# Performance work log

Hardware: AMD Instinct MI355X
Metric: run time of the kernel (lower is better)

Reference implementation:

```python
import jax, jax.numpy as jnp
import numpy as np
import math

B, S, D, H, L, FF = 16, 512, 1024, 16, 4, 4096
DK = D // H
EPS = 1e-5
NEG = -1e32


def make_pe(max_len, d_model):
    pos = np.arange(max_len, dtype=np.float32)[:, None]
    div = np.exp(np.arange(0, d_model, 2, dtype=np.float32) * (-math.log(10000.0) / d_model))
    pe = np.zeros((max_len, d_model), dtype=np.float32)
    pe[:, 0::2] = np.sin(pos * div)
    pe[:, 1::2] = np.cos(pos * div)
    return jnp.asarray(pe[None])  # [1, max_len, d_model]


def setup_inputs() -> dict:
    key = jax.random.key(0)
    ks = jax.random.split(key, 32)
    sd = 0.02
    inp = {
        'q_embed_data': jax.random.normal(ks[0], (B, S, D), jnp.float32),
        'qa_embed_data': jax.random.normal(ks[1], (B, S, D), jnp.float32),
        'forget_rate': jax.random.uniform(ks[2], (B, 1, S, 1), jnp.float32),
        'pe': make_pe(S, D),
        'Wk': jax.random.normal(ks[3], (L, D, D), jnp.float32) * sd,
        'bk': jnp.zeros((L, D), jnp.float32),
        'Wv': jax.random.normal(ks[4], (L, D, D), jnp.float32) * sd,
        'bv': jnp.zeros((L, D), jnp.float32),
        'Wo': jax.random.normal(ks[5], (L, D, D), jnp.float32) * sd,
        'bo': jnp.zeros((L, D), jnp.float32),
        'W1': jax.random.normal(ks[6], (L, D, FF), jnp.float32) * sd,
        'b1': jnp.zeros((L, FF), jnp.float32),
        'W2': jax.random.normal(ks[7], (L, FF, D), jnp.float32) * sd,
        'b2': jnp.zeros((L, D), jnp.float32),
        'ln1_g': jnp.ones((L, D), jnp.float32),
        'ln1_b': jnp.zeros((L, D), jnp.float32),
        'ln2_g': jnp.ones((L, D), jnp.float32),
        'ln2_b': jnp.zeros((L, D), jnp.float32),
    }
    return inp


def layernorm(x, g, b):
    m = jnp.mean(x, -1, keepdims=True)
    v = jnp.mean((x - m) ** 2, -1, keepdims=True)
    return (x - m) * jax.lax.rsqrt(v + EPS) * g + b


def forward(q_embed_data, qa_embed_data, forget_rate, pe,
            Wk, bk, Wv, bv, Wo, bo, W1, b1, W2, b2,
            ln1_g, ln1_b, ln2_g, ln2_b):
    x = q_embed_data + pe[:, :S]
    y = qa_embed_data + pe[:, :S]
    # mask==0 path: allowed positions are strictly below diagonal (j < i)
    allowed = jnp.tril(jnp.ones((S, S), bool), k=-1)
    scale = 1.0 / math.sqrt(DK)
    for l in range(L):
        # kq_same: q also uses k_linear
        k = (x @ Wk[l] + bk[l]).reshape(B, S, H, DK).transpose(0, 2, 1, 3)
        q = k
        v = (y @ Wv[l] + bv[l]).reshape(B, S, H, DK).transpose(0, 2, 1, 3)
        scores = jnp.einsum('bhid,bhjd->bhij', q, k) * scale
        scores = scores * forget_rate  # [B,1,S,1] broadcasts over heads/cols
        scores = jnp.where(allowed, scores, NEG)
        attn = jax.nn.softmax(scores, axis=-1)
        attn = attn.at[:, :, 0, :].set(0.0)  # zero_pad of first query row
        out = jnp.einsum('bhij,bhjd->bhid', attn, v)
        out = out.transpose(0, 2, 1, 3).reshape(B, S, D) @ Wo[l] + bo[l]
        x = layernorm(x + out, ln1_g[l], ln1_b[l])
        ff = jax.nn.relu(x @ W1[l] + b1[l]) @ W2[l] + b2[l]
        x = layernorm(x + ff, ln2_g[l], ln2_b[l])
    return x


def reference(q_embed_data, qa_embed_data, forget_rate, pe,
              Wk, bk, Wv, bv, Wo, bo, W1, b1, W2, b2,
              ln1_g, ln1_b, ln2_g, ln2_b):
    return forward(q_embed_data, qa_embed_data, forget_rate, pe,
                   Wk, bk, Wv, bv, Wo, bo, W1, b1, W2, b2,
                   ln1_g, ln1_b, ln2_g, ln2_b)
```

## Files before the change

kernel.cpp:

```cpp
#include <hip/hip_runtime.h>
#include <hip/hip_bf16.h>
#include <cstdint>
#include <cstddef>

#define Bq 16
#define Sq 512
#define Dq 1024
#define Hq 16
#define Lq 4
#define FFq 4096
#define Mq (Bq * Sq)

typedef unsigned short ushort_t;
typedef __attribute__((ext_vector_type(8))) short short8;
typedef __attribute__((ext_vector_type(8))) unsigned short ushortx8;
typedef __attribute__((ext_vector_type(4))) unsigned short ushortx4;
typedef __attribute__((ext_vector_type(4))) float floatx4;
typedef __attribute__((ext_vector_type(16))) float floatx16;

__device__ __forceinline__ float bf2f(ushort_t u) {
  union { unsigned int i; float f; } x;
  x.i = ((unsigned int)u) << 16;
  return x.f;
}
__device__ __forceinline__ ushort_t f2bf(float f) {
  unsigned int u = __float_as_uint(f);
  u += 0x7fffu + ((u >> 16) & 1u);
  return (ushort_t)(u >> 16);
}

#define GLL16(gp, lp) __builtin_amdgcn_global_load_lds( \
    (__attribute__((address_space(1))) void*)(gp),      \
    (__attribute__((address_space(3))) void*)(lp), 16, 0, 0)

__global__ void probe_kernel(const ushort_t* __restrict__ pe,
                             const ushort_t* __restrict__ g1,
                             int* __restrict__ flags)
{
  if (threadIdx.x == 0 && blockIdx.x == 0) {
    flags[0] = (pe[1] == (ushort_t)0x3F80u) ? 1 : 0;
    flags[1] = (g1[0] == (ushort_t)0x3F80u) ? 1 : 0;
  }
}

struct CvtArgs {
  const void* src[10];
  ushort_t*   dst[10];
  int         n[10];
  int         fi[10];
  int         cum[11];
};
__global__ __launch_bounds__(256) void convert_all_kernel(
    CvtArgs a, const int* __restrict__ flags)
{
  const int bidx = blockIdx.x;
  int s = 0;
  while (s < 9 && bidx >= a.cum[s + 1]) ++s;
  const int i = (bidx - a.cum[s]) * 256 + threadIdx.x;
  if (i >= a.n[s]) return;
  if (flags[a.fi[s]]) a.dst[s][i] = ((const ushort_t*)a.src[s])[i];
  else                a.dst[s][i] = f2bf(((const float*)a.src[s])[i]);
}

__global__ __launch_bounds__(256, 4) void gemm128_kernel(
    const ushort_t* __restrict__ A0, const ushort_t* __restrict__ BT0,
    const ushort_t* __restrict__ bias0, ushort_t* __restrict__ C0, int koff0,
    const ushort_t* __restrict__ A1, const ushort_t* __restrict__ BT1,
    const ushort_t* __restrict__ bias1, ushort_t* __restrict__ C1, int koff1,
    int N, int Kst, int Klen, int relu)
{
  __shared__ __align__(16) ushort_t As[2][128 * 32];
  __shared__ __align__(16) ushort_t Bs[2][128 * 32];

  const ushort_t* A    = blockIdx.z ? A1 : A0;
  const ushort_t* BT   = blockIdx.z ? BT1 : BT0;
  const ushort_t* bias = blockIdx.z ? bias1 : bias0;
  ushort_t*       C    = blockIdx.z ? C1 : C0;
  const int       koff = blockIdx.z ? koff1 : koff0;

  const int t = threadIdx.x;
  const int l = t & 63;
  const int wid = t >> 6;
  const int l31 = l & 31;
  const int wr = wid >> 1;
  const int wc = wid & 1;

  int bx = blockIdx.x, by = blockIdx.y;
  {
    const int gx = gridDim.x, gy = gridDim.y;
    if ((gy & 7) == 0) {
      const int orig = by * gx + bx;
      const int xcd = orig & 7;
      const int local = orig >> 3;
      const int rows = gy >> 3;
      by = xcd * rows + local % rows;
      bx = local / rows;
    }
  }
  const long m0 = (long)by * 128;
  const long n0 = (long)bx * 128;
  const int nk = Klen >> 5;

  const int rA = t >> 2;
  const int scol = (((t & 3) ^ ((rA >> 1) & 3)) << 3);
  const ushort_t* sA = A + (m0 + rA) * (long)Kst + koff + scol;
  const ushort_t* sB = BT + (n0 + rA) * (long)Kst + koff + scol;
  const long rs64 = 64L * (long)Kst;
  const int lws = wid * 512;

#define STG(buf_, kt_) do {                                            \
    const long ko_ = (long)(kt_) << 5;                                 \
    GLL16(sA + ko_,        &As[(buf_)][lws]);                          \
    GLL16(sA + rs64 + ko_, &As[(buf_)][2048 + lws]);                   \
    GLL16(sB + ko_,        &Bs[(buf_)][lws]);                          \
    GLL16(sB + rs64 + ko_, &Bs[(buf_)][2048 + lws]);                   \
  } while (0)

  floatx16 acc[2][2];
#pragma unroll
  for (int i = 0; i < 2; ++i)
#pragma unroll
    for (int j = 0; j < 2; ++j)
#pragma unroll
      for (int r = 0; r < 16; ++r) acc[i][j][r] = 0.0f;

  const int xo = (l >> 1) & 3;
  const int co0 = (((l >> 5)) ^ xo) << 3;
  const int co1 = ((2 + (l >> 5)) ^ xo) << 3;
  const int arow = wr * 64 + l31;
  const int brow = wc * 64 + l31;

  STG(0, 0);
  __syncthreads();

  for (int kt = 0; kt < nk; ++kt) {
    const int buf = kt & 1;
    if (kt + 1 < nk) STG(buf ^ 1, kt + 1);

    short8 a[2][2], b[2][2];
#pragma unroll
    for (int fr = 0; fr < 2; ++fr) {
      a[fr][0] = *(const short8*)&As[buf][(arow + fr * 32) * 32 + co0];
      a[fr][1] = *(const short8*)&As[buf][(arow + fr * 32) * 32 + co1];
    }
#pragma unroll
    for (int fc = 0; fc < 2; ++fc) {
      b[fc][0] = *(const short8*)&Bs[buf][(brow + fc * 32) * 32 + co0];
      b[fc][1] = *(const short8*)&Bs[buf][(brow + fc * 32) * 32 + co1];
    }

#pragma unroll
    for (int sl = 0; sl < 2; ++sl)
#pragma unroll
      for (int fc = 0; fc < 2; ++fc)
#pragma unroll
        for (int fr = 0; fr < 2; ++fr)
          acc[fr][fc] = __builtin_amdgcn_mfma_f32_32x32x16_bf16(
              a[fr][sl], b[fc][sl], acc[fr][fc], 0, 0, 0);

    __syncthreads();
  }
#undef STG

#pragma unroll
  for (int fc = 0; fc < 2; ++fc) {
    const long col = n0 + wc * 64 + fc * 32 + l31;
    const float bsv = bias ? bf2f(bias[col]) : 0.0f;
#pragma unroll
    for (int fr = 0; fr < 2; ++fr) {
      const floatx16 v = acc[fr][fc];
      const long rbase = m0 + wr * 64 + fr * 32 + 4 * (l >> 5);
#pragma unroll
      for (int r = 0; r < 16; ++r) {
        const long row = rbase + (r & 3) + 8 * (r >> 2);
        float x = v[r] + bsv;
        if (relu) x = fmaxf(x, 0.0f);
        C[row * N + col] = f2bf(x);
      }
    }
  }
}

__global__ __launch_bounds__(256) void attn_kernel(
    const ushort_t* __restrict__ kq, const ushort_t* __restrict__ vt,
    const ushort_t* __restrict__ fr, ushort_t* __restrict__ ao)
{
  __shared__ __align__(16) ushort_t P[4][64 * 72];
  const int t = threadIdx.x;
  const int lane = t & 63;
  const int w4 = t >> 6;
  const int wq = blockIdx.y * 4 + w4;
  const int b = blockIdx.x >> 4;
  const int h = blockIdx.x & 15;
  const int la = lane & 15;
  const int lb = lane >> 4;
  const int i0 = wq * 64;
  const long kbase = ((long)b * Sq) * Dq + h * 64;
  const long vbase = ((long)(b * Hq + h)) * (64L * Sq);

  short8 qf[4][2];
#pragma unroll
  for (int mf = 0; mf < 4; ++mf)
#pragma unroll
    for (int tt = 0; tt < 2; ++tt)
      qf[mf][tt] = *(const short8*)&kq[kbase + (long)(i0 + mf * 16 + la) * Dq + tt * 32 + lb * 8];

  float frs[4][4];
#pragma unroll
  for (int mf = 0; mf < 4; ++mf)
#pragma unroll
    for (int r = 0; r < 4; ++r)
      frs[mf][r] = 0.125f * bf2f(fr[b * Sq + i0 + mf * 16 + lb * 4 + r]);

  const floatx4 z4 = {0.f, 0.f, 0.f, 0.f};
  floatx4 o[4][4];
  float mrun[4][4], lrun[4][4];
#pragma unroll
  for (int mf = 0; mf < 4; ++mf)
#pragma unroll
    for (int x = 0; x < 4; ++x) {
      o[mf][x] = z4;
      mrun[mf][x] = -1e30f;
      lrun[mf][x] = 0.0f;
    }

  for (int jt = 0; jt <= wq; ++jt) {
    const int j0 = jt * 64;
    floatx4 s[4][4];
#pragma unroll
    for (int mf = 0; mf < 4; ++mf)
#pragma unroll
      for (int jf = 0; jf < 4; ++jf) s[mf][jf] = z4;

#pragma unroll
    for (int tt = 0; tt < 2; ++tt) {
      short8 kf[4];
#pragma unroll
      for (int jf = 0; jf < 4; ++jf)
        kf[jf] = *(const short8*)&kq[kbase + (long)(j0 + jf * 16 + la) * Dq + tt * 32 + lb * 8];
#pragma unroll
      for (int mf = 0; mf < 4; ++mf)
#pragma unroll
        for (int jf = 0; jf < 4; ++jf)
          s[mf][jf] = __builtin_amdgcn_mfma_f32_16x16x32_bf16(qf[mf][tt], kf[jf], s[mf][jf], 0, 0, 0);
    }

    const bool diag = (jt == wq);
#pragma unroll
    for (int mf = 0; mf < 4; ++mf)
#pragma unroll
      for (int jf = 0; jf < 4; ++jf)
#pragma unroll
        for (int r = 0; r < 4; ++r) {
          float x = s[mf][jf][r] * frs[mf][r];
          if (diag && (j0 + jf * 16 + la) >= (i0 + mf * 16 + lb * 4 + r)) x = -1e30f;
          s[mf][jf][r] = x;
        }

#pragma unroll
    for (int mf = 0; mf < 4; ++mf)
#pragma unroll
      for (int r = 0; r < 4; ++r) {
        float pm = fmaxf(fmaxf(s[mf][0][r], s[mf][1][r]), fmaxf(s[mf][2][r], s[mf][3][r]));
        pm = fmaxf(pm, __shfl_xor(pm, 1));
        pm = fmaxf(pm, __shfl_xor(pm, 2));
        pm = fmaxf(pm, __shfl_xor(pm, 4));
        pm = fmaxf(pm, __shfl_xor(pm, 8));
        const float mo = mrun[mf][r];
        const float mn = fmaxf(mo, pm);
        const float sc = __expf(mo - mn);
        mrun[mf][r] = mn;
        float rs = 0.0f;
#pragma unroll
        for (int jf = 0; jf < 4; ++jf) {
          const float p = __expf(s[mf][jf][r] - mn);
          s[mf][jf][r] = p;
          rs += p;
        }
        rs += __shfl_xor(rs, 1);
        rs += __shfl_xor(rs, 2);
        rs += __shfl_xor(rs, 4);
        rs += __shfl_xor(rs, 8);
        lrun[mf][r] = lrun[mf][r] * sc + rs;
#pragma unroll
        for (int df = 0; df < 4; ++df) o[mf][df][r] *= sc;
      }

#pragma unroll
    for (int mf = 0; mf < 4; ++mf)
#pragma unroll
      for (int jf = 0; jf < 4; ++jf)
#pragma unroll
        for (int r = 0; r < 4; ++r)
          P[w4][(mf * 16 + lb * 4 + r) * 72 + jf * 16 + la] = f2bf(s[mf][jf][r]);

#pragma unroll
    for (int tt = 0; tt < 2; ++tt) {
      short8 pf[4], vf[4];
#pragma unroll
      for (int mf = 0; mf < 4; ++mf)
        pf[mf] = *(const short8*)&P[w4][(mf * 16 + la) * 72 + tt * 32 + lb * 8];
#pragma unroll
      for (int df = 0; df < 4; ++df)
        vf[df] = *(const short8*)&vt[vbase + (long)(df * 16 + la) * Sq + j0 + tt * 32 + lb * 8];
#pragma unroll
      for (int mf = 0; mf < 4; ++mf)
#pragma unroll
        for (int df = 0; df < 4; ++df)
          o[mf][df] = __builtin_amdgcn_mfma_f32_16x16x32_bf16(pf[mf], vf[df], o[mf][df], 0, 0, 0);
    }
  }

#pragma unroll
  for (int mf = 0; mf < 4; ++mf)
#pragma unroll
    for (int df = 0; df < 4; ++df)
#pragma unroll
      for (int r = 0; r < 4; ++r) {
        const int ii = i0 + mf * 16 + lb * 4 + r;
        const float vv = (ii == 0) ? 0.0f : o[mf][df][r] / lrun[mf][r];
        ao[((long)b * Sq + ii) * Dq + h * 64 + df * 16 + la] = f2bf(vv);
      }
}

__global__ __launch_bounds__(256) void ln_kernel(
    float* __restrict__ xf, const ushort_t* __restrict__ add,
    const ushort_t* __restrict__ add2,
    const ushort_t* __restrict__ g, const ushort_t* __restrict__ bb,
    ushort_t* __restrict__ outb, float* __restrict__ outf,
    const int* __restrict__ flags, int final_)
{
  __shared__ float red[2][4];
  const long row = blockIdx.x;
  const int t = threadIdx.x;
  const int c = t * 4;
  float* xr = xf + row * Dq;
  const ushort_t* ar = add + row * Dq;

  floatx4 xv = *(floatx4*)&xr[c];
  ushortx4 av = *(const ushortx4*)&ar[c];
  ushortx4 a2v;
  if (add2) a2v = *(const ushortx4*)&add2[row * Dq + c];
  float v[4];
  float s1 = 0.f, s2 = 0.f;
#pragma unroll
  for (int e = 0; e < 4; ++e) {
    float av_ = bf2f(av[e]);
    if (add2) av_ += bf2f(a2v[e]);
    v[e] = xv[e] + av_;
    s1 += v[e];
    s2 += v[e] * v[e];
  }
#pragma unroll
  for (int m = 1; m < 64; m <<= 1) {
    s1 += __shfl_xor(s1, m);
    s2 += __shfl_xor(s2, m);
  }
  const int lane = t & 63, w = t >> 6;
  if (lane == 0) { red[0][w] = s1; red[1][w] = s2; }
  __syncthreads();
  s1 = red[0][0] + red[0][1] + red[0][2] + red[0][3];
  s2 = red[1][0] + red[1][1] + red[1][2] + red[1][3];
  const float mean = s1 * (1.0f / Dq);
  const float var = fmaxf(s2 * (1.0f / Dq) - mean * mean, 0.0f);
  const float rstd = rsqrtf(var + 1e-5f);
  ushortx4 gv = *(const ushortx4*)&g[c];
  ushortx4 bv = *(const ushortx4*)&bb[c];
  ushortx4 ob;
  floatx4 xo;
#pragma unroll
  for (int e = 0; e < 4; ++e) {
    const float y = (v[e] - mean) * rstd * bf2f(gv[e]) + bf2f(bv[e]);
    xo[e] = y;
    ob[e] = f2bf(y);
  }
  *(floatx4*)&xr[c] = xo;
  if (final_ && !flags[0]) {
    *(floatx4*)&outf[row * Dq + c] = xo;
  } else {
    *(ushortx4*)&outb[row * Dq + c] = ob;
  }
}

__global__ __launch_bounds__(256) void addpe_kernel(
    const void* __restrict__ qe, const void* __restrict__ qa,
    const void* __restrict__ pe, float* __restrict__ xf,
    ushort_t* __restrict__ xb, ushort_t* __restrict__ yb,
    const int* __restrict__ flags)
{
  const long i = ((long)blockIdx.x * 256 + threadIdx.x) * 8;
  const long sd = i & ((long)Sq * Dq - 1);
  const bool isb = flags[0] != 0;
  float q[8], a[8], p[8];
  if (isb) {
    ushortx8 q8 = *(const ushortx8*)((const ushort_t*)qe + i);
    ushortx8 a8 = *(const ushortx8*)((const ushort_t*)qa + i);
    ushortx8 p8 = *(const ushortx8*)((const ushort_t*)pe + sd);
#pragma unroll
    for (int e = 0; e < 8; ++e) { q[e] = bf2f(q8[e]); a[e] = bf2f(a8[e]); p[e] = bf2f(p8[e]); }
  } else {
    const float* qp = (const float*)qe + i;
    const float* ap = (const float*)qa + i;
    const float* pp = (const float*)pe + sd;
    floatx4 q0 = *(const floatx4*)qp, q1 = *(const floatx4*)(qp + 4);
    floatx4 a0 = *(const floatx4*)ap, a1 = *(const floatx4*)(ap + 4);
    floatx4 p0 = *(const floatx4*)pp, p1 = *(const floatx4*)(pp + 4);
#pragma unroll
    for (int e = 0; e < 4; ++e) {
      q[e] = q0[e]; q[e + 4] = q1[e];
      a[e] = a0[e]; a[e + 4] = a1[e];
      p[e] = p0[e]; p[e + 4] = p1[e];
    }
  }
  ushortx8 xo, yo;
  floatx4 f0, f1;
#pragma unroll
  for (int e = 0; e < 8; ++e) {
    const float xvv = (isb ? q[e] : bf2f(f2bf(q[e]))) + (isb ? p[e] : bf2f(f2bf(p[e])));
    const float yvv = (isb ? a[e] : bf2f(f2bf(a[e]))) + (isb ? p[e] : bf2f(f2bf(p[e])));
    if (e < 4) { f0[e] = xvv; } else { f1[e - 4] = xvv; }
    xo[e] = f2bf(xvv);
    yo[e] = f2bf(yvv);
  }
  *(floatx4*)&xf[i] = f0;
  *(floatx4*)&xf[i + 4] = f1;
  *(ushortx8*)&xb[i] = xo;
  *(ushortx8*)&yb[i] = yo;
}

__global__ __launch_bounds__(256) void transpose_kernel(
    const void* __restrict__ src, ushort_t* __restrict__ dst, int K, int N,
    const int* __restrict__ flags)
{
  __shared__ __align__(16) ushort_t tile[64][72];
  const bool isb = flags[1] != 0;
  const long base = (long)blockIdx.z * K * N;
  const int k0 = blockIdx.y * 64, n0 = blockIdx.x * 64;
  const int t = threadIdx.x;
  const int r = t >> 3;
  const int cc = (t & 7) << 3;
#pragma unroll
  for (int it = 0; it < 2; ++it) {
    const int rr = r + it * 32;
    const long gi = base + (long)(k0 + rr) * N + n0 + cc;
    if (isb) {
      *(short8*)&tile[rr][cc] = *(const short8*)((const ushort_t*)src + gi);
    } else {
      const float* sf = (const float*)src + gi;
      floatx4 v0 = *(const floatx4*)sf;
      floatx4 v1 = *(const floatx4*)(sf + 4);
#pragma unroll
      for (int e = 0; e < 4; ++e) {
        tile[rr][cc + e] = f2bf(v0[e]);
        tile[rr][cc + 4 + e] = f2bf(v1[e]);
      }
    }
  }
  __syncthreads();
#pragma unroll
  for (int it = 0; it < 2; ++it) {
    const int rr = r + it * 32;
    short8 v;
#pragma unroll
    for (int e = 0; e < 8; ++e) v[e] = (short)tile[cc + e][rr];
    *(short8*)&dst[base + (long)(n0 + rr) * K + k0 + cc] = v;
  }
}

__global__ __launch_bounds__(256) void vtrans_kernel(
    const ushort_t* __restrict__ vb, ushort_t* __restrict__ vt)
{
  __shared__ __align__(16) ushort_t tile[64][72];
  const int b = blockIdx.y >> 4, h = blockIdx.y & 15;
  const int j0 = blockIdx.x * 64;
  const int t = threadIdx.x;
  const int r = t >> 3;
  const int cc = (t & 7) << 3;
#pragma unroll
  for (int it = 0; it < 2; ++it) {
    const int rr = r + it * 32;
    *(short8*)&tile[rr][cc] = *(const short8*)&vb[((long)b * Sq + j0 + rr) * Dq + h * 64 + cc];
  }
  __syncthreads();
#pragma unroll
  for (int it = 0; it < 2; ++it) {
    const int rr = r + it * 32;
    short8 v;
#pragma unroll
    for (int e = 0; e < 8; ++e) v[e] = (short)tile[cc + e][rr];
    *(short8*)&vt[((long)(b * Hq + h) * 64 + rr) * Sq + j0 + cc] = v;
  }
}

extern "C" void kernel_launch(void* const* d_in, const int* in_sizes, int n_in,
                              void* d_out, int out_size, void* d_ws, size_t ws_size,
                              hipStream_t stream)
{
  if (n_in < 18) return;
  const void* qe  = d_in[0];
  const void* qa  = d_in[1];
  const void* fr  = d_in[2];
  const void* pe  = d_in[3];
  const void* Wk  = d_in[4];
  const void* bk  = d_in[5];
  const void* Wv  = d_in[6];
  const void* bv  = d_in[7];
  const void* Wo  = d_in[8];
  const void* bo  = d_in[9];
  const void* W1  = d_in[10];
  const void* b1  = d_in[11];
  const void* W2  = d_in[12];
  const void* b2  = d_in[13];
  const void* g1  = d_in[14];
  const void* be1 = d_in[15];
  const void* g2  = d_in[16];
  const void* be2 = d_in[17];

  char* ws = (char*)d_ws;
  const size_t SM = 243269632L;
  const size_t NEED = SM + 114752L;
  if (ws_size < NEED) return;

  float*    xf   = (float*)   (ws + 0L);
  ushort_t* xb   = (ushort_t*)(ws + 33554432L);
  ushort_t* yb   = (ushort_t*)(ws + 50331648L);
  ushort_t* tmpD = (ushort_t*)(ws + 67108864L);
  ushort_t* WkT  = (ushort_t*)(ws + 83886080L);
  ushort_t* WvT  = (ushort_t*)(ws + 92274688L);
  ushort_t* WoT  = (ushort_t*)(ws + 100663296L);
  ushort_t* W1T  = (ushort_t*)(ws + 109051904L);
  ushort_t* W2T  = (ushort_t*)(ws + 142606336L);
  ushort_t* kb   = (ushort_t*)(ws + 176160768L);
  ushort_t* vbf  = (ushort_t*)(ws + 192937984L);
  ushort_t* vtb  = (ushort_t*)(ws + 209715200L);
  ushort_t* ff1  = kb;

  int*      flags = (int*)(ws + SM);
  ushort_t* frc  = (ushort_t*)(ws + SM + 64);
  ushort_t* bkc  = (ushort_t*)(ws + SM + 16448);
  ushort_t* bvc  = (ushort_t*)(ws + SM + 24640);
  ushort_t* boc  = (ushort_t*)(ws + SM + 32832);
  ushort_t* b1c  = (ushort_t*)(ws + SM + 41024);
  ushort_t* b2c  = (ushort_t*)(ws + SM + 73792);
  ushort_t* g1c  = (ushort_t*)(ws + SM + 81984);
  ushort_t* be1c = (ushort_t*)(ws + SM + 90176);
  ushort_t* g2c  = (ushort_t*)(ws + SM + 98368);
  ushort_t* be2c = (ushort_t*)(ws + SM + 106560);

  probe_kernel<<<1, 64, 0, stream>>>((const ushort_t*)pe, (const ushort_t*)g1, flags);

  {
    CvtArgs a;
    const void* srcs[10] = {fr, bk, bv, bo, b1, b2, g1, be1, g2, be2};
    ushort_t*   dsts[10] = {frc, bkc, bvc, boc, b1c, b2c, g1c, be1c, g2c, be2c};
    const int   ns[10]   = {8192, 4096, 4096, 4096, 16384, 4096, 4096, 4096, 4096, 4096};
    int cum = 0;
    for (int s = 0; s < 10; ++s) {
      a.src[s] = srcs[s]; a.dst[s] = dsts[s]; a.n[s] = ns[s];
      a.fi[s] = (s == 0) ? 0 : 1;
      a.cum[s] = cum;
      cum += (ns[s] + 255) / 256;
    }
    a.cum[10] = cum;
    convert_all_kernel<<<cum, 256, 0, stream>>>(a, flags);
  }

  transpose_kernel<<<dim3(16, 16, 4), 256, 0, stream>>>(Wk, WkT, 1024, 1024, flags);
  transpose_kernel<<<dim3(16, 16, 4), 256, 0, stream>>>(Wv, WvT, 1024, 1024, flags);
  transpose_kernel<<<dim3(16, 16, 4), 256, 0, stream>>>(Wo, WoT, 1024, 1024, flags);
  transpose_kernel<<<dim3(64, 16, 4), 256, 0, stream>>>(W1, W1T, 1024, 4096, flags);
  transpose_kernel<<<dim3(16, 64, 4), 256, 0, stream>>>(W2, W2T, 4096, 1024, flags);

  addpe_kernel<<<4096, 256, 0, stream>>>(qe, qa, pe, xf, xb, yb, flags);

  for (int l = 0; l < 4; ++l) {
    gemm128_kernel<<<dim3(8, 64, 2), 256, 0, stream>>>(
        xb, WkT + (long)l * 1048576, bkc + l * 1024, kb, 0,
        yb, WvT + (long)l * 1048576, bvc + l * 1024, vbf, 0,
        1024, 1024, 1024, 0);
    vtrans_kernel<<<dim3(8, 256), 256, 0, stream>>>(vbf, vtb);
    attn_kernel<<<dim3(256, 2), 256, 0, stream>>>(kb, vtb, frc, vbf);
    gemm128_kernel<<<dim3(8, 64, 2), 256, 0, stream>>>(
        vbf, WoT + (long)l * 1048576, boc + l * 1024, tmpD, 0,
        vbf, WoT + (long)l * 1048576, nullptr,        xb,   512,
        1024, 1024, 512, 0);
    ln_kernel<<<8192, 256, 0, stream>>>(xf, tmpD, xb, g1c + l * 1024, be1c + l * 1024,
                                        xb, nullptr, flags, 0);
    gemm128_kernel<<<dim3(32, 64, 1), 256, 0, stream>>>(
        xb, W1T + (long)l * 4194304, b1c + l * 4096, ff1, 0,
        xb, W1T + (long)l * 4194304, b1c + l * 4096, ff1, 0,
        4096, 1024, 1024, 1);
    gemm128_kernel<<<dim3(8, 64, 2), 256, 0, stream>>>(
        ff1, W2T + (long)l * 4194304, b2c + l * 1024, tmpD, 0,
        ff1, W2T + (long)l * 4194304, nullptr,        xb,   2048,
        1024, 4096, 2048, 0);
    if (l == 3) {
      ln_kernel<<<8192, 256, 0, stream>>>(xf, tmpD, xb, g2c + l * 1024, be2c + l * 1024,
                                          (ushort_t*)d_out, (float*)d_out, flags, 1);
    } else {
      ln_kernel<<<8192, 256, 0, stream>>>(xf, tmpD, xb, g2c + l * 1024, be2c + l * 1024,
                                          xb, nullptr, flags, 0);
    }
  }
}
```

Baseline: 1.641 ms.

## Enlarge GEMM tile to 256x128 with triple-buffered LDS pipeline

The GEMM kernel now computes a 256x128 output tile per block instead of 128x128, with each wave holding 4x2 MFMA accumulators. Double buffering with __syncthreads becomes a three-stage LDS pipeline that uses explicit vmcnt waits and raw s_barrier, so loads for two tiles ahead overlap compute. The aim is more reuse per LDS load and better hiding of global latency. In exchange there are more registers and more LDS per block, occupancy drops to 2 blocks per CU, and the grids shrink to half as many blocks, which may leave CUs underfilled on the smaller GEMMs.

```diff
diff --git a/kernel.cpp b/kernel.cpp
--- a/kernel.cpp
+++ b/kernel.cpp
@@ -32,6 +32,12 @@
 #define GLL16(gp, lp) __builtin_amdgcn_global_load_lds( \
     (__attribute__((address_space(1))) void*)(gp),      \
     (__attribute__((address_space(3))) void*)(lp), 16, 0, 0)
+
+template<int N> __device__ __forceinline__ void waitvm() {
+  if constexpr (N == 0)       asm volatile("s_waitcnt vmcnt(0)" ::: "memory");
+  else if constexpr (N == 6)  asm volatile("s_waitcnt vmcnt(6)" ::: "memory");
+  else                        asm volatile("s_waitcnt vmcnt(12)" ::: "memory");
+}
 
 __global__ void probe_kernel(const ushort_t* __restrict__ pe,
                              const ushort_t* __restrict__ g1,
@@ -62,15 +68,15 @@
   else                a.dst[s][i] = f2bf(((const float*)a.src[s])[i]);
 }
 
-__global__ __launch_bounds__(256, 4) void gemm128_kernel(
+__global__ __launch_bounds__(256, 2) void gemm256_kernel(
     const ushort_t* __restrict__ A0, const ushort_t* __restrict__ BT0,
     const ushort_t* __restrict__ bias0, ushort_t* __restrict__ C0, int koff0,
     const ushort_t* __restrict__ A1, const ushort_t* __restrict__ BT1,
     const ushort_t* __restrict__ bias1, ushort_t* __restrict__ C1, int koff1,
     int N, int Kst, int Klen, int relu)
 {
-  __shared__ __align__(16) ushort_t As[2][128 * 32];
-  __shared__ __align__(16) ushort_t Bs[2][128 * 32];
+  __shared__ __align__(16) ushort_t As[3][256 * 32];
+  __shared__ __align__(16) ushort_t Bs[3][128 * 32];
 
   const ushort_t* A    = blockIdx.z ? A1 : A0;
   const ushort_t* BT   = blockIdx.z ? BT1 : BT0;
@@ -97,28 +103,30 @@
       bx = local / rows;
     }
   }
-  const long m0 = (long)by * 128;
+  const long m0 = (long)by * 256;
   const long n0 = (long)bx * 128;
   const int nk = Klen >> 5;
 
-  const int rA = t >> 2;
-  const int scol = (((t & 3) ^ ((rA >> 1) & 3)) << 3);
-  const ushort_t* sA = A + (m0 + rA) * (long)Kst + koff + scol;
-  const ushort_t* sB = BT + (n0 + rA) * (long)Kst + koff + scol;
+  const int srow = t >> 2;
+  const int scol = (((t & 3) ^ ((srow >> 1) & 3)) << 3);
+  const ushort_t* sA = A + (m0 + srow) * (long)Kst + koff + scol;
+  const ushort_t* sB = BT + (n0 + srow) * (long)Kst + koff + scol;
   const long rs64 = 64L * (long)Kst;
   const int lws = wid * 512;
 
 #define STG(buf_, kt_) do {                                            \
     const long ko_ = (long)(kt_) << 5;                                 \
-    GLL16(sA + ko_,        &As[(buf_)][lws]);                          \
-    GLL16(sA + rs64 + ko_, &As[(buf_)][2048 + lws]);                   \
-    GLL16(sB + ko_,        &Bs[(buf_)][lws]);                          \
-    GLL16(sB + rs64 + ko_, &Bs[(buf_)][2048 + lws]);                   \
+    GLL16(sA + ko_,            &As[(buf_)][lws]);                      \
+    GLL16(sA + rs64 + ko_,     &As[(buf_)][2048 + lws]);               \
+    GLL16(sA + 2 * rs64 + ko_, &As[(buf_)][4096 + lws]);               \
+    GLL16(sA + 3 * rs64 + ko_, &As[(buf_)][6144 + lws]);               \
+    GLL16(sB + ko_,            &Bs[(buf_)][lws]);                      \
+    GLL16(sB + rs64 + ko_,     &Bs[(buf_)][2048 + lws]);               \
   } while (0)
 
-  floatx16 acc[2][2];
-#pragma unroll
-  for (int i = 0; i < 2; ++i)
+  floatx16 acc[4][2];
+#pragma unroll
+  for (int i = 0; i < 4; ++i)
 #pragma unroll
     for (int j = 0; j < 2; ++j)
 #pragma unroll
@@ -127,19 +135,23 @@
   const int xo = (l >> 1) & 3;
   const int co0 = (((l >> 5)) ^ xo) << 3;
   const int co1 = ((2 + (l >> 5)) ^ xo) << 3;
-  const int arow = wr * 64 + l31;
+  const int arow = wr * 128 + l31;
   const int brow = wc * 64 + l31;
 
   STG(0, 0);
-  __syncthreads();
+  if (nk > 1) STG(1, 1);
 
   for (int kt = 0; kt < nk; ++kt) {
-    const int buf = kt & 1;
-    if (kt + 1 < nk) STG(buf ^ 1, kt + 1);
-
-    short8 a[2][2], b[2][2];
-#pragma unroll
-    for (int fr = 0; fr < 2; ++fr) {
+    const int buf = kt % 3;
+    if (kt + 2 < nk) { STG((kt + 2) % 3, kt + 2); waitvm<12>(); }
+    else if (kt + 1 < nk) waitvm<6>();
+    else waitvm<0>();
+    __builtin_amdgcn_s_barrier();
+    __builtin_amdgcn_sched_barrier(0);
+
+    short8 a[4][2], b[2][2];
+#pragma unroll
+    for (int fr = 0; fr < 4; ++fr) {
       a[fr][0] = *(const short8*)&As[buf][(arow + fr * 32) * 32 + co0];
       a[fr][1] = *(const short8*)&As[buf][(arow + fr * 32) * 32 + co1];
     }
@@ -154,11 +166,11 @@
 #pragma unroll
       for (int fc = 0; fc < 2; ++fc)
 #pragma unroll
-        for (int fr = 0; fr < 2; ++fr)
+        for (int fr = 0; fr < 4; ++fr)
           acc[fr][fc] = __builtin_amdgcn_mfma_f32_32x32x16_bf16(
               a[fr][sl], b[fc][sl], acc[fr][fc], 0, 0, 0);
 
-    __syncthreads();
+    __builtin_amdgcn_s_barrier();
   }
 #undef STG
 
@@ -167,9 +179,9 @@
     const long col = n0 + wc * 64 + fc * 32 + l31;
     const float bsv = bias ? bf2f(bias[col]) : 0.0f;
 #pragma unroll
-    for (int fr = 0; fr < 2; ++fr) {
+    for (int fr = 0; fr < 4; ++fr) {
       const floatx16 v = acc[fr][fc];
-      const long rbase = m0 + wr * 64 + fr * 32 + 4 * (l >> 5);
+      const long rbase = m0 + wr * 128 + fr * 32 + 4 * (l >> 5);
 #pragma unroll
       for (int r = 0; r < 16; ++r) {
         const long row = rbase + (r & 3) + 8 * (r >> 2);
@@ -574,23 +586,23 @@
   addpe_kernel<<<4096, 256, 0, stream>>>(qe, qa, pe, xf, xb, yb, flags);
 
   for (int l = 0; l < 4; ++l) {
-    gemm128_kernel<<<dim3(8, 64, 2), 256, 0, stream>>>(
+    gemm256_kernel<<<dim3(8, 32, 2), 256, 0, stream>>>(
         xb, WkT + (long)l * 1048576, bkc + l * 1024, kb, 0,
         yb, WvT + (long)l * 1048576, bvc + l * 1024, vbf, 0,
         1024, 1024, 1024, 0);
     vtrans_kernel<<<dim3(8, 256), 256, 0, stream>>>(vbf, vtb);
     attn_kernel<<<dim3(256, 2), 256, 0, stream>>>(kb, vtb, frc, vbf);
-    gemm128_kernel<<<dim3(8, 64, 2), 256, 0, stream>>>(
+    gemm256_kernel<<<dim3(8, 32, 2), 256, 0, stream>>>(
         vbf, WoT + (long)l * 1048576, boc + l * 1024, tmpD, 0,
         vbf, WoT + (long)l * 1048576, nullptr,        xb,   512,
         1024, 1024, 512, 0);
     ln_kernel<<<8192, 256, 0, stream>>>(xf, tmpD, xb, g1c + l * 1024, be1c + l * 1024,
                                         xb, nullptr, flags, 0);
-    gemm128_kernel<<<dim3(32, 64, 1), 256, 0, stream>>>(
+    gemm256_kernel<<<dim3(32, 32, 1), 256, 0, stream>>>(
         xb, W1T + (long)l * 4194304, b1c + l * 4096, ff1, 0,
         xb, W1T + (long)l * 4194304, b1c + l * 4096, ff1, 0,
         4096, 1024, 1024, 1);
-    gemm128_kernel<<<dim3(8, 64, 2), 256, 0, stream>>>(
+    gemm256_kernel<<<dim3(8, 32, 2), 256, 0, stream>>>(
         ff1, W2T + (long)l * 4194304, b2c + l * 1024, tmpD, 0,
         ff1, W2T + (long)l * 4194304, nullptr,        xb,   2048,
         1024, 4096, 2048, 0);
```

Result: no change. 1.624 ms (-1.1%).
